# Kernel optimization log

Hardware: AMD Instinct MI355X
Metric: run time of the kernel (lower is better)

## Reference

```python
import jax, jax.numpy as jnp
import numpy as np

T, HID = 4096, 7168
QL, KVL, ROPE, NOPE, H = 1536, 512, 64, 128, 16
N0 = KVL + ROPE + QL            # 2112, fused qkv_a out (kv first, q second after reorder)
NQ = H * (NOPE + ROPE)          # 3072
SLOTS = 16384
EPS = 1e-6


def rmsnorm(x, g, b):
    v = jnp.mean(x * x, axis=-1, keepdims=True)
    return x * jax.lax.rsqrt(v + EPS) * g + b


def quant_i8(x, scale, offset):
    # per-tensor asymmetric quant: round(x/scale) + offset, clipped to int8
    return jnp.clip(jnp.round(x / scale + offset), -128, 127).astype(jnp.int8)


def rope_half(x, cos, sin):
    # channels are pre-reshuffled by trans_rope_weight to [even..., odd...] half format
    d = x.shape[-1] // 2
    rot = jnp.concatenate([-x[..., d:], x[..., :d]], axis=-1)
    return x * cos + rot * sin


def setup_inputs() -> dict:
    key = jax.random.key(0)
    ks = jax.random.split(key, 12)
    hidden_states = jax.random.normal(ks[0], (T, HID), dtype=jnp.float32)
    wdqkv = jax.random.randint(ks[1], (N0, HID), -64, 64).astype(jnp.int8)
    wuq = jax.random.randint(ks[2], (NQ, QL), -64, 64).astype(jnp.int8)
    descale0 = jax.random.uniform(ks[3], (N0,), dtype=jnp.float32) * 1e-4 + 1e-4
    descale1 = jax.random.uniform(ks[4], (NQ,), dtype=jnp.float32) * 1e-4 + 1e-4
    bias0 = jax.random.randint(ks[5], (N0,), -10, 10).astype(jnp.int32)
    bias1 = jax.random.randint(ks[6], (NQ,), -10, 10).astype(jnp.int32)
    gamma1 = 1.0 + 0.02 * jax.random.normal(ks[7], (QL,), dtype=jnp.float32)
    beta1 = 0.01 * jax.random.normal(ks[8], (QL,), dtype=jnp.float32)
    gamma2 = 1.0 + 0.02 * jax.random.normal(ks[9], (KVL,), dtype=jnp.float32)
    w_kc = 0.02 * jax.random.normal(ks[10], (H, NOPE, KVL), dtype=jnp.float32)
    # rotary tables in half (neox) layout: [cos(a), cos(a)] over rope/2 freqs
    pos = jnp.arange(T, dtype=jnp.float32)
    inv_freq = 1.0 / (10000.0 ** (jnp.arange(ROPE // 2, dtype=jnp.float32) / (ROPE // 2)))
    ang = pos[:, None] * inv_freq[None, :]
    cos = jnp.concatenate([jnp.cos(ang), jnp.cos(ang)], axis=-1)
    sin = jnp.concatenate([jnp.sin(ang), jnp.sin(ang)], axis=-1)
    return {
        'hidden_states': hidden_states,
        'gamma0': jnp.ones((HID,), jnp.float32),
        'beta0': jnp.zeros((HID,), jnp.float32),
        'wdqkv': wdqkv,
        'descale0': descale0,
        'bias0': bias0,
        'quant_scale0': jnp.full((1,), 0.05, jnp.float32),
        'quant_offset0': jnp.full((1,), 3, jnp.int32),
        'gamma1': gamma1,
        'beta1': beta1,
        'wuq': wuq,
        'descale1': descale1,
        'bias1': bias1,
        'quant_scale1': jnp.full((1,), 0.05, jnp.float32),
        'quant_offset1': jnp.full((1,), 3, jnp.int32),
        'gamma2': gamma2,
        'cos': cos,
        'sin': sin,
        'w_kc': w_kc,
        'kv_cache': jnp.zeros((SLOTS, 1, KVL), jnp.float32),
        'kv_cache_rope': jnp.zeros((SLOTS, 1, ROPE), jnp.float32),
        'slot_mapping': jnp.arange(T, dtype=jnp.int32),
    }


def reference(hidden_states, gamma0, beta0, wdqkv, descale0, bias0, quant_scale0,
              quant_offset0, gamma1, beta1, wuq, descale1, bias1, quant_scale1,
              quant_offset1, gamma2, cos, sin, w_kc, kv_cache, kv_cache_rope,
              slot_mapping):
    # --- stage 0: rmsnorm + per-tensor quant + int8 GEMM (fused qkv_a) ---
    x = rmsnorm(hidden_states, gamma0, beta0)
    x8 = quant_i8(x, quant_scale0, quant_offset0.astype(jnp.float32))
    acc0 = jnp.matmul(x8.astype(jnp.int32), wdqkv.astype(jnp.int32).T)
    out0 = (acc0 + bias0).astype(jnp.float32) * descale0        # [T, N0]

    ckv = out0[:, :KVL]                                          # kv latent
    k_rope = out0[:, KVL:KVL + ROPE]                             # rope part (pre-reshuffled)
    q_lat = out0[:, KVL + ROPE:]                                 # q latent

    # --- kv path: rmsnorm latent, rope key, scatter into caches ---
    ckv_n = rmsnorm(ckv, gamma2, 0.0)
    k_rope = rope_half(k_rope, cos, sin)
    kv_cache = kv_cache.at[slot_mapping, 0, :].set(ckv_n)
    kv_cache_rope = kv_cache_rope.at[slot_mapping, 0, :].set(k_rope)

    # --- q path: rmsnorm + quant + int8 GEMM (q_b) + rope + absorb w_kc ---
    qn = rmsnorm(q_lat, gamma1, beta1)
    q8 = quant_i8(qn, quant_scale1, quant_offset1.astype(jnp.float32))
    acc1 = jnp.matmul(q8.astype(jnp.int32), wuq.astype(jnp.int32).T)
    q = ((acc1 + bias1).astype(jnp.float32) * descale1).reshape(T, H, NOPE + ROPE)
    q_nope = q[..., :NOPE]
    q_rope_out = rope_half(q[..., NOPE:], cos[:, None, :], sin[:, None, :])
    # absorbed projection onto kv latent space: [T,H,nope] x [H,nope,kvl]
    q_nope_out = jnp.einsum('thn,hnk->thk', q_nope, w_kc)
    return (q_rope_out, kv_cache_rope, q_nope_out, kv_cache)
```

## Files before the change

kernel.cpp:

```cpp
#include <hip/hip_runtime.h>
#include <hip/hip_bf16.h>
#include <stdint.h>

#define T_TOK 4096
#define HID   7168
#define N0    2112
#define N0P   2176
#define QL    1536
#define KVL   512
#define ROPE  64
#define NQ    3072
#define H     16
#define NOPE  128
#define SLOTS 16384

#define N40 ((N0 * HID) / 4)
#define N41 ((NQ * QL) / 4)
#define NWKC (H * KVL * NOPE)

typedef int   v4i __attribute__((ext_vector_type(4)));
typedef short v8s __attribute__((ext_vector_type(8)));
typedef float v4f __attribute__((ext_vector_type(4)));

typedef const __attribute__((address_space(1))) void g_void_t;
typedef __attribute__((address_space(3))) void lds_void_t;

__device__ __forceinline__ void gload16(const void* gp, void* lp) {
    __builtin_amdgcn_global_load_lds((g_void_t*)gp, (lds_void_t*)lp, 16, 0, 0);
}

__device__ __forceinline__ int quanti(float v, float qs, float qo) {
    float r = rintf(v / qs + qo);
    r = fminf(127.f, fmaxf(-128.f, r));
    return (int)r;
}

__device__ __forceinline__ unsigned int pack4(int a, int b, int c, int d) {
    return (unsigned int)(a & 255) | ((unsigned int)(b & 255) << 8) |
           ((unsigned int)(c & 255) << 16) | ((unsigned int)(d & 255) << 24);
}

__device__ __forceinline__ unsigned short f2bf(float v) {
    __hip_bfloat16 b = __float2bfloat16(v);
    return *reinterpret_cast<unsigned short*>(&b);
}

__global__ __launch_bounds__(256) void prep_all_kernel(
    const int* __restrict__ wdqkv, const int* __restrict__ wuq,
    const float* __restrict__ wkc,
    unsigned int* __restrict__ w0, unsigned int* __restrict__ w1,
    unsigned short* __restrict__ wkcb)
{
    int i = blockIdx.x * 256 + threadIdx.x;
    if (i < N40) {
        int4 v = ((const int4*)wdqkv)[i];
        w0[i] = pack4(v.x, v.y, v.z, v.w);
        return;
    }
    i -= N40;
    if (i < N41) {
        int4 v = ((const int4*)wuq)[i];
        w1[i] = pack4(v.x, v.y, v.z, v.w);
        return;
    }
    i -= N41;
    if (i < NWKC) {
        int n = i & (NOPE - 1);
        int k = (i >> 7) & (KVL - 1);
        int h = i >> 16;
        wkcb[i] = f2bf(wkc[((size_t)h * NOPE + n) * KVL + k]);
    }
}

__global__ __launch_bounds__(256) void rmsq0_kernel(
    const float* __restrict__ x, const float* __restrict__ g, const float* __restrict__ b,
    const float* __restrict__ qs_p, const int* __restrict__ qo_p,
    unsigned int* __restrict__ x8)
{
    __shared__ float red[4];
    const int t = blockIdx.x, tid = threadIdx.x;
    const float4* xr = (const float4*)(x + (size_t)t * HID);
    float4 vs[7];
    float ss = 0.f;
#pragma unroll
    for (int i = 0; i < 7; i++) {
        float4 v = xr[i * 256 + tid];
        vs[i] = v;
        ss += v.x * v.x + v.y * v.y + v.z * v.z + v.w * v.w;
    }
#pragma unroll
    for (int off = 32; off > 0; off >>= 1) ss += __shfl_down(ss, off);
    if ((tid & 63) == 0) red[tid >> 6] = ss;
    __syncthreads();
    float s = red[0] + red[1] + red[2] + red[3];
    float rs = rsqrtf(s / (float)HID + 1e-6f);
    float qs = qs_p[0];
    float qo = (float)qo_p[0];
    const float4* gr = (const float4*)g;
    const float4* br = (const float4*)b;
    unsigned int* orow = x8 + (size_t)t * (HID / 4);
#pragma unroll
    for (int i = 0; i < 7; i++) {
        int j = i * 256 + tid;
        float4 v = vs[i], gg = gr[j], bb = br[j];
        int q0 = quanti(v.x * rs * gg.x + bb.x, qs, qo);
        int q1 = quanti(v.y * rs * gg.y + bb.y, qs, qo);
        int q2 = quanti(v.z * rs * gg.z + bb.z, qs, qo);
        int q3 = quanti(v.w * rs * gg.w + bb.w, qs, qo);
        orow[j] = pack4(q0, q1, q2, q3);
    }
}

__global__ __launch_bounds__(512, 8) void gemm_i8_db_kernel(
    const signed char* __restrict__ A, const signed char* __restrict__ B,
    const int* __restrict__ bias, const float* __restrict__ descale,
    float* __restrict__ C, int M, int N, int Np, int K, int ntn)
{
    __shared__ __align__(16) signed char As[2][128 * 64];
    __shared__ __align__(16) signed char Bs[2][128 * 64];
    const int tid = threadIdx.x;
    const int lane = tid & 63, wid = tid >> 6;
    const int wm = wid >> 2, wn = wid & 3;
    const int r16 = lane & 15, kq = lane >> 4;

    const int nwg = gridDim.x;
    const int q = nwg >> 3, r = nwg & 7;
    const int xcd = blockIdx.x & 7, idx = blockIdx.x >> 3;
    const int wg = (xcd < r ? xcd * (q + 1) : r * (q + 1) + (xcd - r) * q) + idx;
    const int bm = (wg / ntn) * 128, bn = (wg % ntn) * 128;

    const int srow = tid >> 2;
    const int schunk = (tid & 3) ^ ((srow >> 1) & 3);
    const signed char* aSrc = A + (size_t)(bm + srow) * K + schunk * 16;
    const signed char* bSrc = B + (size_t)(bn + srow) * K + schunk * 16;

    auto STAGE = [&](int buf, int k0) {
        gload16(aSrc + k0, As[buf] + wid * 1024);
        gload16(bSrc + k0, Bs[buf] + wid * 1024);
    };

    int aOff[4], bOff[2];
#pragma unroll
    for (int mi = 0; mi < 4; mi++) {
        int ra = wm * 64 + mi * 16 + r16;
        aOff[mi] = ra * 64 + ((kq ^ ((ra >> 1) & 3)) * 16);
    }
#pragma unroll
    for (int ni = 0; ni < 2; ni++) {
        int rb = wn * 32 + ni * 16 + r16;
        bOff[ni] = rb * 64 + ((kq ^ ((rb >> 1) & 3)) * 16);
    }

    v4i acc[4][2];
#pragma unroll
    for (int i = 0; i < 4; i++)
#pragma unroll
        for (int j = 0; j < 2; j++) acc[i][j] = (v4i){0, 0, 0, 0};

    const int KT = K >> 6;
    STAGE(0, 0);
    for (int kt = 0; kt < KT; kt++) {
        const int cur = kt & 1;
        if (kt + 1 < KT) {
            STAGE(cur ^ 1, (kt + 1) << 6);
            asm volatile("s_waitcnt vmcnt(2)" ::: "memory");
        } else {
            asm volatile("s_waitcnt vmcnt(0)" ::: "memory");
        }
        __builtin_amdgcn_s_barrier();
        const signed char* as = As[cur];
        const signed char* bs = Bs[cur];
        v4i a[4], b[2];
#pragma unroll
        for (int mi = 0; mi < 4; mi++) a[mi] = *(const v4i*)(as + aOff[mi]);
#pragma unroll
        for (int ni = 0; ni < 2; ni++) b[ni] = *(const v4i*)(bs + bOff[ni]);
#pragma unroll
        for (int mi = 0; mi < 4; mi++)
#pragma unroll
            for (int ni = 0; ni < 2; ni++)
                acc[mi][ni] = __builtin_amdgcn_mfma_i32_16x16x64_i8(a[mi], b[ni], acc[mi][ni], 0, 0, 0);
        __builtin_amdgcn_s_barrier();
    }

#pragma unroll
    for (int ni = 0; ni < 2; ni++) {
        int col = bn + wn * 32 + ni * 16 + r16;
        int cc = col < N ? col : 0;
        float ds = descale[cc];
        int bv = bias[cc];
#pragma unroll
        for (int mi = 0; mi < 4; mi++) {
            int rowb = bm + wm * 64 + mi * 16 + kq * 4;
#pragma unroll
            for (int rr = 0; rr < 4; rr++) {
                C[(size_t)(rowb + rr) * Np + col] = (float)(acc[mi][ni][rr] + bv) * ds;
            }
        }
    }
}

__global__ __launch_bounds__(512, 8) void gemm1_fused_kernel(
    const signed char* __restrict__ A, const signed char* __restrict__ B,
    const int* __restrict__ bias, const float* __restrict__ descale,
    const float* __restrict__ cs, const float* __restrict__ sn,
    unsigned short* __restrict__ qn, float* __restrict__ qrope,
    int K, int ntn)
{
    __shared__ __align__(16) signed char As[2][128 * 64];
    __shared__ __align__(16) signed char Bs[2][128 * 64];
    const int tid = threadIdx.x;
    const int lane = tid & 63, wid = tid >> 6;
    const int wm = wid >> 1, wn = wid & 1;
    const int r16 = lane & 15, kq = lane >> 4;

    const int nwg = gridDim.x;
    const int q = nwg >> 3, r = nwg & 7;
    const int xcd = blockIdx.x & 7, idx = blockIdx.x >> 3;
    const int wg = (xcd < r ? xcd * (q + 1) : r * (q + 1) + (xcd - r) * q) + idx;
    const int bm = (wg / ntn) * 128, bn = (wg % ntn) * 128;

    const int srow = tid >> 2;
    const int schunk = (tid & 3) ^ ((srow >> 1) & 3);
    const signed char* aSrc = A + (size_t)(bm + srow) * K + schunk * 16;
    const signed char* bSrc = B + (size_t)(bn + srow) * K + schunk * 16;

    auto STAGE = [&](int buf, int k0) {
        gload16(aSrc + k0, As[buf] + wid * 1024);
        gload16(bSrc + k0, Bs[buf] + wid * 1024);
    };

    int aOff[2], bOff[4];
#pragma unroll
    for (int mi = 0; mi < 2; mi++) {
        int ra = wm * 32 + mi * 16 + r16;
        aOff[mi] = ra * 64 + ((kq ^ ((ra >> 1) & 3)) * 16);
    }
#pragma unroll
    for (int ni = 0; ni < 4; ni++) {
        int rb = wn * 64 + ni * 16 + r16;
        bOff[ni] = rb * 64 + ((kq ^ ((rb >> 1) & 3)) * 16);
    }

    v4i acc[2][4];
#pragma unroll
    for (int i = 0; i < 2; i++)
#pragma unroll
        for (int j = 0; j < 4; j++) acc[i][j] = (v4i){0, 0, 0, 0};

    const int KT = K >> 6;
    STAGE(0, 0);
    for (int kt = 0; kt < KT; kt++) {
        const int cur = kt & 1;
        if (kt + 1 < KT) {
            STAGE(cur ^ 1, (kt + 1) << 6);
            asm volatile("s_waitcnt vmcnt(2)" ::: "memory");
        } else {
            asm volatile("s_waitcnt vmcnt(0)" ::: "memory");
        }
        __builtin_amdgcn_s_barrier();
        const signed char* as = As[cur];
        const signed char* bs = Bs[cur];
        v4i a[2], b[4];
#pragma unroll
        for (int mi = 0; mi < 2; mi++) a[mi] = *(const v4i*)(as + aOff[mi]);
#pragma unroll
        for (int ni = 0; ni < 4; ni++) b[ni] = *(const v4i*)(bs + bOff[ni]);
#pragma unroll
        for (int mi = 0; mi < 2; mi++)
#pragma unroll
            for (int ni = 0; ni < 4; ni++)
                acc[mi][ni] = __builtin_amdgcn_mfma_i32_16x16x64_i8(a[mi], b[ni], acc[mi][ni], 0, 0, 0);
        __builtin_amdgcn_s_barrier();
    }

    float v[2][4][4];
#pragma unroll
    for (int ni = 0; ni < 4; ni++) {
        int col = bn + wn * 64 + ni * 16 + r16;
        float ds = descale[col];
        int bv = bias[col];
#pragma unroll
        for (int mi = 0; mi < 2; mi++)
#pragma unroll
            for (int rr = 0; rr < 4; rr++)
                v[mi][ni][rr] = (float)(acc[mi][ni][rr] + bv) * ds;
    }

    const int wincol = bn + wn * 64;
    const int h = wincol / 192;
    const int segb = wincol - h * 192;

    if (segb < 128) {
#pragma unroll
        for (int mi = 0; mi < 2; mi++) {
            int rowb = bm + wm * 32 + mi * 16 + kq * 4;
#pragma unroll
            for (int rr = 0; rr < 4; rr++) {
                int t = rowb + rr;
#pragma unroll
                for (int ni = 0; ni < 4; ni++) {
                    int d = segb + ni * 16 + r16;
                    qn[(size_t)t * (H * NOPE) + h * NOPE + d] = f2bf(v[mi][ni][rr]);
                }
            }
        }
    } else {
#pragma unroll
        for (int mi = 0; mi < 2; mi++) {
            int rowb = bm + wm * 32 + mi * 16 + kq * 4;
#pragma unroll
            for (int rr = 0; rr < 4; rr++) {
                int t = rowb + rr;
                const float* crow = cs + (size_t)t * ROPE;
                const float* srow2 = sn + (size_t)t * ROPE;
                float* orow = qrope + ((size_t)t * H + h) * ROPE;
#pragma unroll
                for (int ni = 0; ni < 2; ni++) {
                    int dp = ni * 16 + r16;
                    float lo = v[mi][ni][rr];
                    float hi = v[mi][ni + 2][rr];
                    orow[dp]      = lo * crow[dp]      - hi * srow2[dp];
                    orow[dp + 32] = hi * crow[dp + 32] + lo * srow2[dp + 32];
                }
            }
        }
    }
}

__global__ __launch_bounds__(256) void post0_kernel(
    const float* __restrict__ out0,
    const float* __restrict__ gamma2,
    const float* __restrict__ gamma1, const float* __restrict__ beta1,
    const float* __restrict__ qs_p, const int* __restrict__ qo_p,
    const float* __restrict__ cs, const float* __restrict__ sn,
    const int* __restrict__ slot_mapping,
    float* __restrict__ out_kv, float* __restrict__ out_kv_rope,
    signed char* __restrict__ q8)
{
    __shared__ float2 red[4];
    const int t = blockIdx.x, tid = threadIdx.x;
    const float* row = out0 + (size_t)t * N0P;
    float c0 = row[tid], c1 = row[256 + tid];
    float ssc = c0 * c0 + c1 * c1;
    float qv[6];
    float ssq = 0.f;
#pragma unroll
    for (int i = 0; i < 6; i++) {
        float v = row[KVL + ROPE + i * 256 + tid];
        qv[i] = v;
        ssq += v * v;
    }
    float a = ssc, b2 = ssq;
#pragma unroll
    for (int off = 32; off > 0; off >>= 1) {
        a += __shfl_down(a, off);
        b2 += __shfl_down(b2, off);
    }
    if ((tid & 63) == 0) red[tid >> 6] = make_float2(a, b2);
    __syncthreads();
    float sc = red[0].x + red[1].x + red[2].x + red[3].x;
    float sq = red[0].y + red[1].y + red[2].y + red[3].y;
    float rsc = rsqrtf(sc / (float)KVL + 1e-6f);
    float rsq = rsqrtf(sq / (float)QL + 1e-6f);
    int slot = slot_mapping[t];
    out_kv[(size_t)slot * KVL + tid]       = c0 * rsc * gamma2[tid];
    out_kv[(size_t)slot * KVL + 256 + tid] = c1 * rsc * gamma2[256 + tid];
    if (tid < 64) {
        float xv = row[KVL + tid];
        float rot = (tid < 32) ? -row[KVL + tid + 32] : row[KVL + tid - 32];
        out_kv_rope[(size_t)slot * ROPE + tid] = xv * cs[t * ROPE + tid] + rot * sn[t * ROPE + tid];
    }
    float qs = qs_p[0], qo = (float)qo_p[0];
    signed char* q8r = q8 + (size_t)t * QL;
#pragma unroll
    for (int i = 0; i < 6; i++) {
        int j = i * 256 + tid;
        q8r[j] = (signed char)quanti(qv[i] * rsq * gamma1[j] + beta1[j], qs, qo);
    }
}

__global__ __launch_bounds__(256, 2) void gemm_wkc_kernel(
    const unsigned short* __restrict__ Aq,
    const unsigned short* __restrict__ Bw,
    float* __restrict__ out)
{
    __shared__ __align__(16) unsigned short Qs[128 * 128];
    __shared__ __align__(16) unsigned short Ws[128 * 128];
    const int tid = threadIdx.x;
    const int lane = tid & 63, wid = tid >> 6;
    const int wk = wid >> 1, wt = wid & 1;
    const int r16 = lane & 15, kq = lane >> 4;

    const int bt = blockIdx.x * 128;
    const int bk = blockIdx.y * 128;
    const int h  = blockIdx.z;

    {
        const int lr = lane >> 4;
        const int lc = lane & 15;
#pragma unroll
        for (int p = 0; p < 8; p++) {
            int rr = wid * 32 + p * 4 + lr;
            int src_c = lc ^ (rr & 15);
            gload16(Aq + (size_t)(bt + rr) * (H * NOPE) + h * NOPE + src_c * 8,
                    (char*)Qs + (wid * 32 + p * 4) * 256 + lane * 16);
            gload16(Bw + ((size_t)h * KVL + bk + rr) * NOPE + src_c * 8,
                    (char*)Ws + (wid * 32 + p * 4) * 256 + lane * 16);
        }
    }
    asm volatile("s_waitcnt vmcnt(0)" ::: "memory");
    __builtin_amdgcn_s_barrier();

    v4f acc[4][4];
#pragma unroll
    for (int i = 0; i < 4; i++)
#pragma unroll
        for (int j = 0; j < 4; j++) acc[i][j] = (v4f){0.f, 0.f, 0.f, 0.f};

#pragma unroll
    for (int ks = 0; ks < 4; ks++) {
        v8s a[4], b[4];
#pragma unroll
        for (int mi = 0; mi < 4; mi++) {
            int ra = wk * 64 + mi * 16 + r16;
            int ch = (ks * 4 + kq) ^ (ra & 15);
            a[mi] = *(const v8s*)((const char*)Ws + ra * 256 + ch * 16);
        }
#pragma unroll
        for (int ni = 0; ni < 4; ni++) {
            int rb = wt * 64 + ni * 16 + r16;
            int ch = (ks * 4 + kq) ^ (rb & 15);
            b[ni] = *(const v8s*)((const char*)Qs + rb * 256 + ch * 16);
        }
#pragma unroll
        for (int mi = 0; mi < 4; mi++)
#pragma unroll
            for (int ni = 0; ni < 4; ni++)
                acc[mi][ni] = __builtin_amdgcn_mfma_f32_16x16x32_bf16(a[mi], b[ni], acc[mi][ni], 0, 0, 0);
    }

#pragma unroll
    for (int ni = 0; ni < 4; ni++) {
        int t = bt + wt * 64 + ni * 16 + r16;
        float* orow = out + ((size_t)t * H + h) * KVL + bk;
#pragma unroll
        for (int mi = 0; mi < 4; mi++) {
            int k0 = wk * 64 + mi * 16 + kq * 4;
            *(float4*)(orow + k0) = *(float4*)&acc[mi][ni];
        }
    }
}

extern "C" void kernel_launch(void* const* d_in, const int* in_sizes, int n_in,
                              void* d_out, int out_size, void* d_ws, size_t ws_size,
                              hipStream_t stream) {
    const float* hidden   = (const float*)d_in[0];
    const float* gamma0   = (const float*)d_in[1];
    const float* beta0    = (const float*)d_in[2];
    const int*   wdqkv    = (const int*)d_in[3];
    const float* descale0 = (const float*)d_in[4];
    const int*   bias0    = (const int*)d_in[5];
    const float* qs0      = (const float*)d_in[6];
    const int*   qo0      = (const int*)d_in[7];
    const float* gamma1   = (const float*)d_in[8];
    const float* beta1    = (const float*)d_in[9];
    const int*   wuq      = (const int*)d_in[10];
    const float* descale1 = (const float*)d_in[11];
    const int*   bias1    = (const int*)d_in[12];
    const float* qs1      = (const float*)d_in[13];
    const int*   qo1      = (const int*)d_in[14];
    const float* gamma2   = (const float*)d_in[15];
    const float* cos_t    = (const float*)d_in[16];
    const float* sin_t    = (const float*)d_in[17];
    const float* w_kc     = (const float*)d_in[18];
    const int*   slot_map = (const int*)d_in[21];

    float* out_q_rope  = (float*)d_out;
    float* out_kv_rope = out_q_rope + (size_t)T_TOK * H * ROPE;
    float* out_q_nope  = out_kv_rope + (size_t)SLOTS * ROPE;
    float* out_kv      = out_q_nope + (size_t)T_TOK * H * KVL;

    char* ws = (char*)d_ws;
    char* ws_x8 = ws;
    char* ws_w0 = ws_x8 + (size_t)T_TOK * HID;
    char* ws_w1 = ws_w0 + (size_t)N0P * HID;
    unsigned short* ws_wkc = (unsigned short*)(ws_w1 + (size_t)NQ * QL);
    float* ws_out0 = (float*)((char*)ws_wkc + (size_t)H * KVL * NOPE * 2);
    signed char* ws_q8 = (signed char*)((char*)ws_out0 + (size_t)T_TOK * N0P * 4);
    unsigned short* ws_qn = (unsigned short*)((char*)ws_q8 + (size_t)T_TOK * QL);

    hipMemsetAsync(out_kv + (size_t)T_TOK * KVL, 0,
                   (size_t)(SLOTS - T_TOK) * KVL * 4, stream);
    hipMemsetAsync(out_kv_rope + (size_t)T_TOK * ROPE, 0,
                   (size_t)(SLOTS - T_TOK) * ROPE * 4, stream);

    {
        int total = N40 + N41 + NWKC;
        prep_all_kernel<<<(total + 255) / 256, 256, 0, stream>>>(
            wdqkv, wuq, w_kc, (unsigned int*)ws_w0, (unsigned int*)ws_w1, ws_wkc);
    }

    rmsq0_kernel<<<T_TOK, 256, 0, stream>>>(hidden, gamma0, beta0, qs0, qo0, (unsigned int*)ws_x8);

    gemm_i8_db_kernel<<<(T_TOK / 128) * (N0P / 128), 512, 0, stream>>>(
        (const signed char*)ws_x8, (const signed char*)ws_w0, bias0, descale0, ws_out0,
        T_TOK, N0, N0P, HID, N0P / 128);

    post0_kernel<<<T_TOK, 256, 0, stream>>>(ws_out0, gamma2, gamma1, beta1, qs1, qo1,
                                            cos_t, sin_t, slot_map, out_kv, out_kv_rope, ws_q8);

    gemm1_fused_kernel<<<(T_TOK / 128) * (NQ / 128), 512, 0, stream>>>(
        ws_q8, (const signed char*)ws_w1, bias1, descale1, cos_t, sin_t,
        ws_qn, out_q_rope, QL, NQ / 128);

    gemm_wkc_kernel<<<dim3(T_TOK / 128, KVL / 128, H), 256, 0, stream>>>(ws_qn, ws_wkc, out_q_nope);
}
```

Before: 247.1 us.

## Rewrite qkv_a int8 GEMM with 256x128 tiles and triple-buffered phased pipeline

Replaces the double-buffered 128x128x64 int8 GEMM for the first projection with a 256x128 tile, K step of 128, and three LDS stages. Global loads are split across four MFMA phases with barriers and s_setprio so prefetch overlaps compute. Each wave now computes a 64x64 sub-tile, which raises arithmetic intensity per LDS byte. In exchange it uses about 144KB of LDS per block, so only one block fits per CU, which cuts occupancy and the number of workgroups.

```diff
diff --git a/kernel.cpp b/kernel.cpp
--- a/kernel.cpp
+++ b/kernel.cpp
@@ -111,81 +111,158 @@
     }
 }
 
-__global__ __launch_bounds__(512, 8) void gemm_i8_db_kernel(
+__global__ __launch_bounds__(512, 2) void gemm0_8ph_kernel(
     const signed char* __restrict__ A, const signed char* __restrict__ B,
     const int* __restrict__ bias, const float* __restrict__ descale,
     float* __restrict__ C, int M, int N, int Np, int K, int ntn)
 {
-    __shared__ __align__(16) signed char As[2][128 * 64];
-    __shared__ __align__(16) signed char Bs[2][128 * 64];
+    __shared__ __align__(16) signed char LDS[3][49152];
     const int tid = threadIdx.x;
     const int lane = tid & 63, wid = tid >> 6;
-    const int wm = wid >> 2, wn = wid & 3;
+    const int wm = wid >> 1, wn = wid & 1;
     const int r16 = lane & 15, kq = lane >> 4;
 
     const int nwg = gridDim.x;
     const int q = nwg >> 3, r = nwg & 7;
     const int xcd = blockIdx.x & 7, idx = blockIdx.x >> 3;
     const int wg = (xcd < r ? xcd * (q + 1) : r * (q + 1) + (xcd - r) * q) + idx;
-    const int bm = (wg / ntn) * 128, bn = (wg % ntn) * 128;
-
-    const int srow = tid >> 2;
-    const int schunk = (tid & 3) ^ ((srow >> 1) & 3);
-    const signed char* aSrc = A + (size_t)(bm + srow) * K + schunk * 16;
-    const signed char* bSrc = B + (size_t)(bn + srow) * K + schunk * 16;
-
-    auto STAGE = [&](int buf, int k0) {
-        gload16(aSrc + k0, As[buf] + wid * 1024);
-        gload16(bSrc + k0, Bs[buf] + wid * 1024);
-    };
-
-    int aOff[4], bOff[2];
-#pragma unroll
-    for (int mi = 0; mi < 4; mi++) {
-        int ra = wm * 64 + mi * 16 + r16;
-        aOff[mi] = ra * 64 + ((kq ^ ((ra >> 1) & 3)) * 16);
-    }
-#pragma unroll
-    for (int ni = 0; ni < 2; ni++) {
-        int rb = wn * 32 + ni * 16 + r16;
-        bOff[ni] = rb * 64 + ((kq ^ ((rb >> 1) & 3)) * 16);
-    }
-
-    v4i acc[4][2];
+    const int bm = (wg / ntn) * 256, bn = (wg % ntn) * 128;
+
+    const int lr8 = lane >> 3;
+    const int sch = (lane & 7) ^ lr8;
+    const signed char* aSrc = A + (size_t)(bm + wid * 8 + lr8) * K + sch * 16;
+    const signed char* bSrc = B + (size_t)(bn + wid * 8 + lr8) * K + sch * 16;
+
+    int aOff[4][2], bOff[4][2];
+#pragma unroll
+    for (int m = 0; m < 4; m++) {
+        int ra = wm * 64 + m * 16 + r16;
+#pragma unroll
+        for (int kk = 0; kk < 2; kk++)
+            aOff[m][kk] = ra * 128 + (((kk * 4 + kq) ^ (ra & 7)) * 16);
+    }
+#pragma unroll
+    for (int n = 0; n < 4; n++) {
+        int rb = wn * 64 + n * 16 + r16;
+#pragma unroll
+        for (int kk = 0; kk < 2; kk++)
+            bOff[n][kk] = 32768 + rb * 128 + (((kk * 4 + kq) ^ (rb & 7)) * 16);
+    }
+
+    v4i acc[4][4];
 #pragma unroll
     for (int i = 0; i < 4; i++)
 #pragma unroll
-        for (int j = 0; j < 2; j++) acc[i][j] = (v4i){0, 0, 0, 0};
-
-    const int KT = K >> 6;
-    STAGE(0, 0);
+        for (int j = 0; j < 4; j++) acc[i][j] = (v4i){0, 0, 0, 0};
+
+    const int KT = K >> 7;
+
+#pragma unroll
+    for (int p = 0; p < 4; p++) gload16(aSrc + (size_t)(p * 64) * K,       LDS[0] + (p * 8 + wid) * 1024);
+#pragma unroll
+    for (int p = 0; p < 2; p++) gload16(bSrc + (size_t)(p * 64) * K,       LDS[0] + 32768 + (p * 8 + wid) * 1024);
+#pragma unroll
+    for (int p = 0; p < 4; p++) gload16(aSrc + (size_t)(p * 64) * K + 128, LDS[1] + (p * 8 + wid) * 1024);
+#pragma unroll
+    for (int p = 0; p < 2; p++) gload16(bSrc + (size_t)(p * 64) * K + 128, LDS[1] + 32768 + (p * 8 + wid) * 1024);
+    asm volatile("s_waitcnt vmcnt(6)" ::: "memory");
+    __builtin_amdgcn_s_barrier();
+
+    int cur = 0;
     for (int kt = 0; kt < KT; kt++) {
-        const int cur = kt & 1;
-        if (kt + 1 < KT) {
-            STAGE(cur ^ 1, (kt + 1) << 6);
-            asm volatile("s_waitcnt vmcnt(2)" ::: "memory");
+        const signed char* base = LDS[cur];
+        const bool hasNext = (kt + 2 < KT);
+        int sb = cur + 2; if (sb >= 3) sb -= 3;
+        const int k0s = (kt + 2) << 7;
+        signed char* sA = LDS[sb];
+        signed char* sB = LDS[sb] + 32768;
+
+        v4i a0[2][2], a1[2][2], b[4][2];
+
+#pragma unroll
+        for (int m = 0; m < 2; m++)
+#pragma unroll
+            for (int kk = 0; kk < 2; kk++) a0[m][kk] = *(const v4i*)(base + aOff[m][kk]);
+#pragma unroll
+        for (int n = 0; n < 4; n++)
+#pragma unroll
+            for (int kk = 0; kk < 2; kk++) b[n][kk] = *(const v4i*)(base + bOff[n][kk]);
+        if (hasNext) {
+            gload16(aSrc + k0s,                    sA + (0 * 8 + wid) * 1024);
+            gload16(aSrc + k0s + (size_t)64 * K,   sA + (1 * 8 + wid) * 1024);
+        }
+        __builtin_amdgcn_s_barrier();
+        asm volatile("s_waitcnt lgkmcnt(0)" ::: "memory");
+        __builtin_amdgcn_sched_barrier(0);
+        __builtin_amdgcn_s_setprio(1);
+#pragma unroll
+        for (int m = 0; m < 2; m++)
+#pragma unroll
+            for (int n = 0; n < 2; n++)
+#pragma unroll
+                for (int kk = 0; kk < 2; kk++)
+                    acc[m][n] = __builtin_amdgcn_mfma_i32_16x16x64_i8(a0[m][kk], b[n][kk], acc[m][n], 0, 0, 0);
+        __builtin_amdgcn_s_setprio(0);
+        __builtin_amdgcn_s_barrier();
+
+#pragma unroll
+        for (int m = 0; m < 2; m++)
+#pragma unroll
+            for (int kk = 0; kk < 2; kk++) a1[m][kk] = *(const v4i*)(base + aOff[m + 2][kk]);
+        if (hasNext) {
+            gload16(aSrc + k0s + (size_t)128 * K,  sA + (2 * 8 + wid) * 1024);
+            gload16(aSrc + k0s + (size_t)192 * K,  sA + (3 * 8 + wid) * 1024);
+        }
+        __builtin_amdgcn_s_barrier();
+        asm volatile("s_waitcnt lgkmcnt(0)" ::: "memory");
+        __builtin_amdgcn_sched_barrier(0);
+        __builtin_amdgcn_s_setprio(1);
+#pragma unroll
+        for (int m = 0; m < 2; m++)
+#pragma unroll
+            for (int n = 0; n < 2; n++)
+#pragma unroll
+                for (int kk = 0; kk < 2; kk++)
+                    acc[m][n + 2] = __builtin_amdgcn_mfma_i32_16x16x64_i8(a0[m][kk], b[n + 2][kk], acc[m][n + 2], 0, 0, 0);
+        __builtin_amdgcn_s_setprio(0);
+        __builtin_amdgcn_s_barrier();
+
+        if (hasNext) {
+            gload16(bSrc + k0s,                    sB + (0 * 8 + wid) * 1024);
+            gload16(bSrc + k0s + (size_t)64 * K,   sB + (1 * 8 + wid) * 1024);
+            asm volatile("s_waitcnt vmcnt(6)" ::: "memory");
         } else {
             asm volatile("s_waitcnt vmcnt(0)" ::: "memory");
         }
         __builtin_amdgcn_s_barrier();
-        const signed char* as = As[cur];
-        const signed char* bs = Bs[cur];
-        v4i a[4], b[2];
-#pragma unroll
-        for (int mi = 0; mi < 4; mi++) a[mi] = *(const v4i*)(as + aOff[mi]);
-#pragma unroll
-        for (int ni = 0; ni < 2; ni++) b[ni] = *(const v4i*)(bs + bOff[ni]);
-#pragma unroll
-        for (int mi = 0; mi < 4; mi++)
-#pragma unroll
-            for (int ni = 0; ni < 2; ni++)
-                acc[mi][ni] = __builtin_amdgcn_mfma_i32_16x16x64_i8(a[mi], b[ni], acc[mi][ni], 0, 0, 0);
-        __builtin_amdgcn_s_barrier();
-    }
-
-#pragma unroll
-    for (int ni = 0; ni < 2; ni++) {
-        int col = bn + wn * 32 + ni * 16 + r16;
+        __builtin_amdgcn_s_setprio(1);
+#pragma unroll
+        for (int m = 0; m < 2; m++)
+#pragma unroll
+            for (int n = 0; n < 2; n++)
+#pragma unroll
+                for (int kk = 0; kk < 2; kk++)
+                    acc[m + 2][n] = __builtin_amdgcn_mfma_i32_16x16x64_i8(a1[m][kk], b[n][kk], acc[m + 2][n], 0, 0, 0);
+        __builtin_amdgcn_s_setprio(0);
+        __builtin_amdgcn_s_barrier();
+
+        __builtin_amdgcn_s_setprio(1);
+#pragma unroll
+        for (int m = 0; m < 2; m++)
+#pragma unroll
+            for (int n = 0; n < 2; n++)
+#pragma unroll
+                for (int kk = 0; kk < 2; kk++)
+                    acc[m + 2][n + 2] = __builtin_amdgcn_mfma_i32_16x16x64_i8(a1[m][kk], b[n + 2][kk], acc[m + 2][n + 2], 0, 0, 0);
+        __builtin_amdgcn_s_setprio(0);
+        __builtin_amdgcn_s_barrier();
+
+        cur = cur + 1; if (cur >= 3) cur -= 3;
+    }
+
+#pragma unroll
+    for (int ni = 0; ni < 4; ni++) {
+        int col = bn + wn * 64 + ni * 16 + r16;
         int cc = col < N ? col : 0;
         float ds = descale[cc];
         int bv = bias[cc];
@@ -503,7 +580,7 @@
 
     rmsq0_kernel<<<T_TOK, 256, 0, stream>>>(hidden, gamma0, beta0, qs0, qo0, (unsigned int*)ws_x8);
 
-    gemm_i8_db_kernel<<<(T_TOK / 128) * (N0P / 128), 512, 0, stream>>>(
+    gemm0_8ph_kernel<<<(T_TOK / 256) * (N0P / 128), 512, 0, stream>>>(
         (const signed char*)ws_x8, (const signed char*)ws_w0, bias0, descale0, ws_out0,
         T_TOK, N0, N0P, HID, N0P / 128);
 
```

New measurement: 271.6 us. +9.9%, slower.
